# Optimization experiments

Hardware: AMD Instinct MI355X
Metric: run time of the kernel (lower is better)

## Reference

```python
import jax, jax.numpy as jnp
import numpy as np

B, C, H, W = 8, 256, 64, 64
DQK = 16  # int(sqrt(out_channels))


def setup_inputs() -> dict:
    key = jax.random.key(0)
    ks = jax.random.split(key, 8)
    s_in = 1.0 / np.sqrt(C)
    return {
        "x": jax.random.normal(ks[0], (B, C, H, W), dtype=jnp.float32),
        "Wf": jax.random.normal(ks[1], (DQK, C), dtype=jnp.float32) * s_in,
        "bf": jnp.zeros((DQK,), dtype=jnp.float32),
        "Wg": jax.random.normal(ks[2], (DQK, C), dtype=jnp.float32) * s_in,
        "bg": jnp.zeros((DQK,), dtype=jnp.float32),
        "Wh": jax.random.normal(ks[3], (C, C), dtype=jnp.float32) * s_in,
        "bh": jnp.zeros((C,), dtype=jnp.float32),
        # original inits attention_multiplier to 0.0; use small nonzero so output depends on attention path
        "gamma": jnp.float32(0.5),
    }


def reference(x, Wf, bf, Wg, bg, Wh, bh, gamma):
    b, c, h, w = x.shape
    hw = h * w
    # 1x1 convs == per-pixel channel projections
    f = (jnp.einsum('bchw,oc->bohw', x, Wf) + bf[None, :, None, None]).reshape(b, -1, hw)  # [B,DQK,HW]
    g = (jnp.einsum('bchw,oc->bohw', x, Wg) + bg[None, :, None, None]).reshape(b, -1, hw)  # [B,DQK,HW]
    hh = (jnp.einsum('bchw,oc->bohw', x, Wh) + bh[None, :, None, None]).reshape(b, -1, hw)  # [B,C,HW]
    # s[b,n,m] = sum_k g[b,k,n] * f[b,k,m]  -> [B,HW,HW]
    s = jnp.einsum('bkn,bkm->bnm', g, f)
    beta = jax.nn.softmax(s, axis=-1)
    # o = beta @ h^T, then transpose back to channel-first: [B,C,HW]
    o = jnp.einsum('bnm,bcm->bcn', beta, hh)
    return gamma * o.reshape(x.shape) + x
```

## Files before the change

### kernel.cpp

```cpp
#include <hip/hip_runtime.h>
#include <math.h>

#define BATCH 8
#define CH    256
#define HWN   4096
#define DQK   16

typedef __attribute__((ext_vector_type(8))) short short8;
typedef __attribute__((ext_vector_type(4))) float float4v;

#define L2E 1.4426950408889634f

__device__ __forceinline__ unsigned short f2bf(float f) {
    union { float f; unsigned int u; } v; v.f = f;
    unsigned int r = v.u + 0x7FFF + ((v.u >> 16) & 1);
    return (unsigned short)(r >> 16);
}
__device__ __forceinline__ unsigned int cvtpk(float lo, float hi) {
    unsigned int r;
    asm("v_cvt_pk_bf16_f32 %0, %1, %2" : "=v"(r) : "v"(lo), "v"(hi));
    return r;
}
__device__ __forceinline__ float ex2(float x) {
#if __has_builtin(__builtin_amdgcn_exp2f)
    return __builtin_amdgcn_exp2f(x);
#else
    return exp2f(x);
#endif
}
__device__ __forceinline__ int perm_ft(int m) {
    return (m & ~28) | ((m & 24) >> 1) | ((m & 4) << 2);
}

__global__ __launch_bounds__(256) void wcast_kernel(
    const float* __restrict__ Wf, const float* __restrict__ bf_,
    const float* __restrict__ Wg, const float* __restrict__ bg,
    const float* __restrict__ Wh, const float* __restrict__ bh,
    unsigned short* __restrict__ Wbf, float* __restrict__ bcat)
{
    const int r = blockIdx.x;
    const int t = threadIdx.x;
    const float* src = (r < 16) ? (Wf + r*CH) : (r < 32) ? (Wg + (r-16)*CH) : (Wh + (r-32)*CH);
    Wbf[r*CH + t] = f2bf(src[t]);
    if (t == 0) bcat[r] = (r < 16) ? bf_[r] : (r < 32) ? bg[r-16] : bh[r-32];
}

__global__ __launch_bounds__(256) void xt_kernel(const float* __restrict__ x,
                                                 unsigned short* __restrict__ xt)
{
    const int t  = threadIdx.x;
    const int p0 = blockIdx.x * 64;
    const int c0 = blockIdx.y * 64;
    const int b  = blockIdx.z;
    __shared__ unsigned short tile[64][74];
    const int col4 = (t & 15) * 4;
    const int cr   = t >> 4;
    #pragma unroll
    for (int j = 0; j < 4; j++) {
        int c = cr + j*16;
        float4 v = *(const float4*)&x[(size_t)(b*CH + c0 + c)*HWN + p0 + col4];
        unsigned int u01 = cvtpk(v.x, v.y), u23 = cvtpk(v.z, v.w);
        tile[col4+0][c] = (unsigned short)u01;
        tile[col4+1][c] = (unsigned short)(u01 >> 16);
        tile[col4+2][c] = (unsigned short)u23;
        tile[col4+3][c] = (unsigned short)(u23 >> 16);
    }
    __syncthreads();
    const int pr = t >> 2;
    const int cb = (t & 3) * 16;
    unsigned int outv[8];
    #pragma unroll
    for (int i = 0; i < 8; i++)
        outv[i] = *(const unsigned int*)&tile[pr][cb + 2*i];
    unsigned short* dst = &xt[(size_t)(b*HWN + p0 + pr)*CH + c0 + cb];
    *(uint4*)dst       = *(uint4*)&outv[0];
    *(uint4*)(dst + 8) = *(uint4*)&outv[4];
}

__global__ __launch_bounds__(256, 6) void proj_kernel(
    const unsigned short* __restrict__ xt, const unsigned short* __restrict__ Wbf,
    const float* __restrict__ bcat,
    unsigned short* __restrict__ ft, unsigned short* __restrict__ g,
    unsigned short* __restrict__ h3)
{
    const int t      = threadIdx.x;
    const int px0    = blockIdx.x * 64;
    const int b      = blockIdx.y;
    const int rtbase = blockIdx.z * 6;
    const int lane = t & 63, w = t >> 6, l15 = lane & 15, quad = lane >> 4;

    float4v acc[6];
    #pragma unroll
    for (int rt = 0; rt < 6; rt++) acc[rt] = (float4v){0.f,0.f,0.f,0.f};

    const unsigned short* xrow = &xt[((size_t)(b*HWN + px0 + w*16 + l15))*CH + quad*8];
    const unsigned short* wrow = &Wbf[(size_t)l15*CH + quad*8];

    #pragma unroll
    for (int ks = 0; ks < 8; ks++) {
        short8 afrag = *(const short8*)&xrow[ks*32];
        #pragma unroll
        for (int rt = 0; rt < 6; rt++) {
            short8 bfrag = *(const short8*)&wrow[(size_t)(rtbase + rt)*16*CH + ks*32];
            acc[rt] = __builtin_amdgcn_mfma_f32_16x16x32_bf16(afrag, bfrag, acc[rt], 0, 0, 0);
        }
    }

    const int pxl = px0 + w*16 + quad*4;
    const int mt  = (px0 >> 5) + (w >> 1);
    const int sub = ((w & 1)*2 + (quad >> 1))*128 + l15*8 + (quad & 1)*4;
    #pragma unroll
    for (int rt = 0; rt < 6; rt++) {
        const int R = rtbase + rt;
        if (R == 0) {
            float bv = bcat[l15];
            const int s0 = perm_ft(pxl);
            unsigned int p01 = cvtpk((acc[rt][0] + bv)*L2E, (acc[rt][1] + bv)*L2E);
            unsigned int p23 = cvtpk((acc[rt][2] + bv)*L2E, (acc[rt][3] + bv)*L2E);
            unsigned short* fp0 = &ft[((size_t)b*HWN + s0)*32];
            fp0[l15]       = (unsigned short)p01;         fp0[16 + l15]  = 0;
            fp0[32 + l15]  = (unsigned short)(p01 >> 16); fp0[48 + l15]  = 0;
            fp0[64 + l15]  = (unsigned short)p23;         fp0[80 + l15]  = 0;
            fp0[96 + l15]  = (unsigned short)(p23 >> 16); fp0[112 + l15] = 0;
        } else if (R == 1) {
            float bv = bcat[16 + l15];
            unsigned int a01 = cvtpk(acc[rt][0] + bv, acc[rt][1] + bv);
            unsigned int a23 = cvtpk(acc[rt][2] + bv, acc[rt][3] + bv);
            *(uint2*)&g[(size_t)(b*DQK + l15)*HWN + pxl] = make_uint2(a01, a23);
        } else {
            float bv = bcat[R*16 + l15];
            unsigned int u0 = cvtpk(acc[rt][0] + bv, acc[rt][1] + bv);
            unsigned int u1 = cvtpk(acc[rt][2] + bv, acc[rt][3] + bv);
            *(uint2*)&h3[(((size_t)((b*128 + mt)*16 + (R-2))) << 9) + sub] = make_uint2(u0, u1);
        }
    }
}

__global__ __launch_bounds__(512, 4) void attn_kernel(
    const unsigned short* __restrict__ ft, const unsigned short* __restrict__ g,
    const unsigned short* __restrict__ h3, const float* __restrict__ x,
    const float* __restrict__ gamma_p, float* __restrict__ out)
{
    const int t    = threadIdx.x;
    const int b    = blockIdx.x & 7;
    const int q0   = (blockIdx.x >> 3) * 64;
    const int lane = t & 63, w = t >> 6, l15 = lane & 15, quad = lane >> 4;
    const int qt_w = w >> 1, half = w & 1;

    __shared__ __align__(16) uint4 pB[4][2][4][64];
    __shared__ float l_l[4][16][2];

    union { short8 v; unsigned short u[8]; } gfrag;
    #pragma unroll
    for (int j = 0; j < 8; j++) {
        int k = quad*8 + j;
        gfrag.u[j] = (k < DQK) ? g[(size_t)(b*DQK + k)*HWN + q0 + qt_w*16 + l15] : (unsigned short)0;
    }

    const unsigned short* ftb = ft + (size_t)b*HWN*32;
    const unsigned short* h3b = h3 + ((size_t)b << 20);

    short8 fr[2][4];
    float4v acc[2][4];
    #pragma unroll
    for (int i = 0; i < 2; i++)
        #pragma unroll
        for (int j = 0; j < 4; j++) acc[i][j] = (float4v){0.f,0.f,0.f,0.f};
    float l_acc = 0.f;
    uint4 Pa, Pb;

#define EXP2_PACK(sv0, sv1, Pout) do {                                         \
      float e0 = ex2((sv0)[0]), e1 = ex2((sv0)[1]), e2 = ex2((sv0)[2]), e3 = ex2((sv0)[3]); \
      float e4 = ex2((sv1)[0]), e5 = ex2((sv1)[1]), e6 = ex2((sv1)[2]), e7 = ex2((sv1)[3]); \
      l_acc += ((e0 + e1) + (e2 + e3)) + ((e4 + e5) + (e6 + e7));              \
      Pout = make_uint4(cvtpk(e0, e1), cvtpk(e2, e3), cvtpk(e4, e5), cvtpk(e6, e7)); \
    } while (0)

    {
        short8 f0[4];
        #pragma unroll
        for (int j = 0; j < 4; j++)
            f0[j] = *(const short8*)&ftb[(size_t)((j>>1)*64 + (half*2 + (j&1))*16 + l15)*32 + quad*8];
        float4v z = {0.f,0.f,0.f,0.f};
        float4v s0 = __builtin_amdgcn_mfma_f32_16x16x32_bf16(f0[0], gfrag.v, z, 0, 0, 0);
        float4v s1 = __builtin_amdgcn_mfma_f32_16x16x32_bf16(f0[1], gfrag.v, z, 0, 0, 0);
        float4v s2 = __builtin_amdgcn_mfma_f32_16x16x32_bf16(f0[2], gfrag.v, z, 0, 0, 0);
        float4v s3 = __builtin_amdgcn_mfma_f32_16x16x32_bf16(f0[3], gfrag.v, z, 0, 0, 0);
        EXP2_PACK(s0, s1, Pa);
        EXP2_PACK(s2, s3, Pb);
    }
    #pragma unroll
    for (int j = 0; j < 4; j++)
        fr[0][j] = *(const short8*)&ftb[(size_t)((2 + (j>>1))*64 + (half*2 + (j&1))*16 + l15)*32 + quad*8];

#define SUPER(U, T, DO_NEXT) do {                                              \
    pB[(U)*2 + 0][half][qt_w][lane] = Pa;                                      \
    pB[(U)*2 + 1][half][qt_w][lane] = Pb;                                      \
    __syncthreads();                                                           \
    short8 hra[2][2], hrb[2][2];                                               \
    _Pragma("unroll")                                                          \
    for (int grp = 0; grp < 2; grp++) {                                        \
      _Pragma("unroll")                                                        \
      for (int ctl = 0; ctl < 2; ctl++) {                                      \
        hra[grp][ctl] = *(const short8*)&h3b[(((size_t)((4*(T) + grp)*16 + w*2 + ctl)) << 9) + lane*8]; \
        hrb[grp][ctl] = *(const short8*)&h3b[(((size_t)((4*(T) + 2 + grp)*16 + w*2 + ctl)) << 9) + lane*8]; \
      }                                                                        \
    }                                                                          \
    if (DO_NEXT) {                                                             \
      _Pragma("unroll")                                                        \
      for (int j = 0; j < 4; j++) {                                            \
        const int nt = (2*(T) + 4 + (j>>1)) & 63;                              \
        fr[(U)^1][j] = *(const short8*)&ftb[(size_t)(nt*64 + (half*2 + (j&1))*16 + l15)*32 + quad*8]; \
      }                                                                        \
      float4v z = {0.f,0.f,0.f,0.f};                                           \
      float4v s0 = __builtin_amdgcn_mfma_f32_16x16x32_bf16(fr[U][0], gfrag.v, z, 0, 0, 0); \
      float4v s1 = __builtin_amdgcn_mfma_f32_16x16x32_bf16(fr[U][1], gfrag.v, z, 0, 0, 0); \
      float4v s2 = __builtin_amdgcn_mfma_f32_16x16x32_bf16(fr[U][2], gfrag.v, z, 0, 0, 0); \
      float4v s3 = __builtin_amdgcn_mfma_f32_16x16x32_bf16(fr[U][3], gfrag.v, z, 0, 0, 0); \
      EXP2_PACK(s0, s1, Pa);                                                   \
      EXP2_PACK(s2, s3, Pb);                                                   \
    }                                                                          \
    __builtin_amdgcn_s_setprio(1);                                             \
    _Pragma("unroll")                                                          \
    for (int grp = 0; grp < 2; grp++) {                                        \
      _Pragma("unroll")                                                        \
      for (int qt = 0; qt < 4; qt++) {                                         \
        union { uint4 uu; short8 v; } bqa, bqb;                                \
        bqa.uu = pB[(U)*2 + 0][grp][qt][lane];                                 \
        bqb.uu = pB[(U)*2 + 1][grp][qt][lane];                                 \
        _Pragma("unroll")                                                      \
        for (int ctl = 0; ctl < 2; ctl++) {                                    \
          acc[ctl][qt] = __builtin_amdgcn_mfma_f32_16x16x32_bf16(hra[grp][ctl], bqa.v, acc[ctl][qt], 0, 0, 0); \
          acc[ctl][qt] = __builtin_amdgcn_mfma_f32_16x16x32_bf16(hrb[grp][ctl], bqb.v, acc[ctl][qt], 0, 0, 0); \
        }                                                                      \
      }                                                                        \
    }                                                                          \
    __builtin_amdgcn_s_setprio(0);                                             \
  } while (0)

    for (int T = 0; T < 30; T += 2) {
        SUPER(0, T, 1);
        SUPER(1, T + 1, 1);
    }
    SUPER(0, 30, 1);
    SUPER(1, 31, 0);
#undef SUPER
#undef EXP2_PACK

    l_acc += __shfl_xor(l_acc, 16, 64);
    l_acc += __shfl_xor(l_acc, 32, 64);
    if (quad == 0) l_l[qt_w][l15][half] = l_acc;
    __syncthreads();

    const float gamma = *gamma_p;
    float linv[4];
    #pragma unroll
    for (int qt = 0; qt < 4; qt++) linv[qt] = 1.f / (l_l[qt][l15][0] + l_l[qt][l15][1]);
    #pragma unroll
    for (int ctl = 0; ctl < 2; ctl++) {
        #pragma unroll
        for (int r = 0; r < 4; r++) {
            int c = w*32 + ctl*16 + quad*4 + r;
            size_t base = (size_t)(b*CH + c)*HWN + q0;
            #pragma unroll
            for (int qt = 0; qt < 4; qt++) {
                size_t o = base + qt*16 + l15;
                out[o] = gamma * acc[ctl][qt][r] * linv[qt] + x[o];
            }
        }
    }
}

extern "C" void kernel_launch(void* const* d_in, const int* in_sizes, int n_in,
                              void* d_out, int out_size, void* d_ws, size_t ws_size,
                              hipStream_t stream) {
    const float* x     = (const float*)d_in[0];
    const float* Wf    = (const float*)d_in[1];
    const float* bf_   = (const float*)d_in[2];
    const float* Wg    = (const float*)d_in[3];
    const float* bg    = (const float*)d_in[4];
    const float* Wh    = (const float*)d_in[5];
    const float* bh    = (const float*)d_in[6];
    const float* gamma = (const float*)d_in[7];
    float* out = (float*)d_out;

    unsigned short* xt   = (unsigned short*)d_ws;
    unsigned short* ftp  = xt  + (size_t)BATCH*HWN*CH;
    unsigned short* g    = ftp + (size_t)BATCH*HWN*32;
    unsigned short* h3   = g   + (size_t)BATCH*DQK*HWN;
    unsigned short* Wbf  = h3  + (size_t)BATCH*128*16*512;
    float*          bcat = (float*)(Wbf + 288*CH);

    wcast_kernel<<<dim3(288), 256, 0, stream>>>(Wf, bf_, Wg, bg, Wh, bh, Wbf, bcat);
    xt_kernel<<<dim3(HWN/64, CH/64, BATCH), 256, 0, stream>>>(x, xt);
    proj_kernel<<<dim3(HWN/64, BATCH, 3), 256, 0, stream>>>(xt, Wbf, bcat, ftp, g, h3);
    attn_kernel<<<dim3((HWN/64)*BATCH), 512, 0, stream>>>(ftp, g, h3, x, gamma, out);
}
```

Measured before the change: 253.6 us.

## Split attention super-step into two half-phases to overlap QK score with PV MFMAs

Restructures the main attention loop so that each super-step runs two half-phases. Each half-phase loads only half of the h tiles and half of the f tiles, and computes the next score/exp tile between the PV MFMAs of the current buffer. This lowers register pressure (fewer live h and f fragments) and interleaves the QK, exp and PV work at finer granularity. It also replaces __syncthreads with a custom barrier that waits only for LDS counters and lets global loads stay in flight. The risks are a subtle ordering change in the prefetch indices and the LDS buffer reuse, which leans on the single barrier per super-step.

Measured after the change: 220.4 us. 13.1% less time.

```diff
diff --git a/kernel.cpp b/kernel.cpp
--- a/kernel.cpp
+++ b/kernel.cpp
@@ -27,6 +27,10 @@
 #else
     return exp2f(x);
 #endif
+}
+__device__ __forceinline__ void lds_barrier() {
+    asm volatile("s_waitcnt lgkmcnt(0)" ::: "memory");
+    __builtin_amdgcn_s_barrier();
 }
 __device__ __forceinline__ int perm_ft(int m) {
     return (m & ~28) | ((m & 24) >> 1) | ((m & 4) << 2);
@@ -160,7 +164,7 @@
     const unsigned short* ftb = ft + (size_t)b*HWN*32;
     const unsigned short* h3b = h3 + ((size_t)b << 20);
 
-    short8 fr[2][4];
+    short8 frE[2], frO[2];
     float4v acc[2][4];
     #pragma unroll
     for (int i = 0; i < 2; i++)
@@ -177,74 +181,91 @@
     } while (0)
 
     {
-        short8 f0[4];
-        #pragma unroll
-        for (int j = 0; j < 4; j++)
-            f0[j] = *(const short8*)&ftb[(size_t)((j>>1)*64 + (half*2 + (j&1))*16 + l15)*32 + quad*8];
+        short8 f0[2];
         float4v z = {0.f,0.f,0.f,0.f};
+        #pragma unroll
+        for (int j = 0; j < 2; j++)
+            f0[j] = *(const short8*)&ftb[(size_t)((half*2 + j)*16 + l15)*32 + quad*8];
         float4v s0 = __builtin_amdgcn_mfma_f32_16x16x32_bf16(f0[0], gfrag.v, z, 0, 0, 0);
         float4v s1 = __builtin_amdgcn_mfma_f32_16x16x32_bf16(f0[1], gfrag.v, z, 0, 0, 0);
-        float4v s2 = __builtin_amdgcn_mfma_f32_16x16x32_bf16(f0[2], gfrag.v, z, 0, 0, 0);
-        float4v s3 = __builtin_amdgcn_mfma_f32_16x16x32_bf16(f0[3], gfrag.v, z, 0, 0, 0);
         EXP2_PACK(s0, s1, Pa);
-        EXP2_PACK(s2, s3, Pb);
-    }
-    #pragma unroll
-    for (int j = 0; j < 4; j++)
-        fr[0][j] = *(const short8*)&ftb[(size_t)((2 + (j>>1))*64 + (half*2 + (j&1))*16 + l15)*32 + quad*8];
-
-#define SUPER(U, T, DO_NEXT) do {                                              \
-    pB[(U)*2 + 0][half][qt_w][lane] = Pa;                                      \
-    pB[(U)*2 + 1][half][qt_w][lane] = Pb;                                      \
-    __syncthreads();                                                           \
-    short8 hra[2][2], hrb[2][2];                                               \
-    _Pragma("unroll")                                                          \
-    for (int grp = 0; grp < 2; grp++) {                                        \
-      _Pragma("unroll")                                                        \
-      for (int ctl = 0; ctl < 2; ctl++) {                                      \
-        hra[grp][ctl] = *(const short8*)&h3b[(((size_t)((4*(T) + grp)*16 + w*2 + ctl)) << 9) + lane*8]; \
-        hrb[grp][ctl] = *(const short8*)&h3b[(((size_t)((4*(T) + 2 + grp)*16 + w*2 + ctl)) << 9) + lane*8]; \
-      }                                                                        \
-    }                                                                          \
-    if (DO_NEXT) {                                                             \
-      _Pragma("unroll")                                                        \
-      for (int j = 0; j < 4; j++) {                                            \
-        const int nt = (2*(T) + 4 + (j>>1)) & 63;                              \
-        fr[(U)^1][j] = *(const short8*)&ftb[(size_t)(nt*64 + (half*2 + (j&1))*16 + l15)*32 + quad*8]; \
-      }                                                                        \
-      float4v z = {0.f,0.f,0.f,0.f};                                           \
-      float4v s0 = __builtin_amdgcn_mfma_f32_16x16x32_bf16(fr[U][0], gfrag.v, z, 0, 0, 0); \
-      float4v s1 = __builtin_amdgcn_mfma_f32_16x16x32_bf16(fr[U][1], gfrag.v, z, 0, 0, 0); \
-      float4v s2 = __builtin_amdgcn_mfma_f32_16x16x32_bf16(fr[U][2], gfrag.v, z, 0, 0, 0); \
-      float4v s3 = __builtin_amdgcn_mfma_f32_16x16x32_bf16(fr[U][3], gfrag.v, z, 0, 0, 0); \
-      EXP2_PACK(s0, s1, Pa);                                                   \
-      EXP2_PACK(s2, s3, Pb);                                                   \
-    }                                                                          \
+        #pragma unroll
+        for (int j = 0; j < 2; j++)
+            f0[j] = *(const short8*)&ftb[(size_t)(64 + (half*2 + j)*16 + l15)*32 + quad*8];
+        s0 = __builtin_amdgcn_mfma_f32_16x16x32_bf16(f0[0], gfrag.v, z, 0, 0, 0);
+        s1 = __builtin_amdgcn_mfma_f32_16x16x32_bf16(f0[1], gfrag.v, z, 0, 0, 0);
+        EXP2_PACK(s0, s1, Pb);
+    }
+    #pragma unroll
+    for (int j = 0; j < 2; j++)
+        frE[j] = *(const short8*)&ftb[(size_t)(2*64 + (half*2 + j)*16 + l15)*32 + quad*8];
+
+#define PV_PHASE(buf, hrv) do {                                                \
     __builtin_amdgcn_s_setprio(1);                                             \
     _Pragma("unroll")                                                          \
     for (int grp = 0; grp < 2; grp++) {                                        \
       _Pragma("unroll")                                                        \
       for (int qt = 0; qt < 4; qt++) {                                         \
-        union { uint4 uu; short8 v; } bqa, bqb;                                \
-        bqa.uu = pB[(U)*2 + 0][grp][qt][lane];                                 \
-        bqb.uu = pB[(U)*2 + 1][grp][qt][lane];                                 \
-        _Pragma("unroll")                                                      \
-        for (int ctl = 0; ctl < 2; ctl++) {                                    \
-          acc[ctl][qt] = __builtin_amdgcn_mfma_f32_16x16x32_bf16(hra[grp][ctl], bqa.v, acc[ctl][qt], 0, 0, 0); \
-          acc[ctl][qt] = __builtin_amdgcn_mfma_f32_16x16x32_bf16(hrb[grp][ctl], bqb.v, acc[ctl][qt], 0, 0, 0); \
-        }                                                                      \
+        union { uint4 uu; short8 v; } bq;                                      \
+        bq.uu = pB[buf][grp][qt][lane];                                        \
+        _Pragma("unroll")                                                      \
+        for (int ctl = 0; ctl < 2; ctl++)                                      \
+          acc[ctl][qt] = __builtin_amdgcn_mfma_f32_16x16x32_bf16(hrv[grp][ctl], bq.v, acc[ctl][qt], 0, 0, 0); \
       }                                                                        \
     }                                                                          \
     __builtin_amdgcn_s_setprio(0);                                             \
   } while (0)
 
+#define SUPER(b0, b1, T, DO_NEXT) do {                                         \
+    pB[b0][half][qt_w][lane] = Pa;                                             \
+    pB[b1][half][qt_w][lane] = Pb;                                             \
+    lds_barrier();                                                             \
+    {                                          \
+      short8 hr[2][2];                                                         \
+      _Pragma("unroll")                                                        \
+      for (int grp = 0; grp < 2; grp++)                                        \
+        _Pragma("unroll")                                                      \
+        for (int ctl = 0; ctl < 2; ctl++)                                      \
+          hr[grp][ctl] = *(const short8*)&h3b[(((size_t)((4*(T) + grp)*16 + w*2 + ctl)) << 9) + lane*8]; \
+      if (DO_NEXT) {                                                           \
+        _Pragma("unroll")                                                      \
+        for (int j = 0; j < 2; j++)                                            \
+          frO[j] = *(const short8*)&ftb[(size_t)((2*(T) + 3)*64 + (half*2 + j)*16 + l15)*32 + quad*8]; \
+        float4v z = {0.f,0.f,0.f,0.f};                                         \
+        float4v s0 = __builtin_amdgcn_mfma_f32_16x16x32_bf16(frE[0], gfrag.v, z, 0, 0, 0); \
+        float4v s1 = __builtin_amdgcn_mfma_f32_16x16x32_bf16(frE[1], gfrag.v, z, 0, 0, 0); \
+        EXP2_PACK(s0, s1, Pa);                                                 \
+      }                                                                        \
+      PV_PHASE(b0, hr);                                                        \
+    }                                                                          \
+    {                                        \
+      short8 hr[2][2];                                                         \
+      _Pragma("unroll")                                                        \
+      for (int grp = 0; grp < 2; grp++)                                        \
+        _Pragma("unroll")                                                      \
+        for (int ctl = 0; ctl < 2; ctl++)                                      \
+          hr[grp][ctl] = *(const short8*)&h3b[(((size_t)((4*(T) + 2 + grp)*16 + w*2 + ctl)) << 9) + lane*8]; \
+      if (DO_NEXT) {                                                           \
+        _Pragma("unroll")                                                      \
+        for (int j = 0; j < 2; j++)                                            \
+          frE[j] = *(const short8*)&ftb[(size_t)((2*(T) + 4)*64 + (half*2 + j)*16 + l15)*32 + quad*8]; \
+        float4v z = {0.f,0.f,0.f,0.f};                                         \
+        float4v s0 = __builtin_amdgcn_mfma_f32_16x16x32_bf16(frO[0], gfrag.v, z, 0, 0, 0); \
+        float4v s1 = __builtin_amdgcn_mfma_f32_16x16x32_bf16(frO[1], gfrag.v, z, 0, 0, 0); \
+        EXP2_PACK(s0, s1, Pb);                                                 \
+      }                                                                        \
+      PV_PHASE(b1, hr);                                                        \
+    }                                                                          \
+  } while (0)
+
     for (int T = 0; T < 30; T += 2) {
-        SUPER(0, T, 1);
-        SUPER(1, T + 1, 1);
-    }
-    SUPER(0, 30, 1);
-    SUPER(1, 31, 0);
+        SUPER(0, 1, T, 1);
+        SUPER(2, 3, T + 1, 1);
+    }
+    SUPER(0, 1, 30, 1);
+    SUPER(2, 3, 31, 0);
 #undef SUPER
+#undef PV_PHASE
 #undef EXP2_PACK
 
     l_acc += __shfl_xor(l_acc, 16, 64);
```
